# Kernel optimization log

Measured on AMD Instinct MI355X. Metric: run time of the kernel, lower is better.

The kernel has to match this reference:

```python
import jax, jax.numpy as jnp
import numpy as np

N = 50000
E = 800000
C_IN = 128
C_HID = 256
C_OUT = 128


def _glorot(key, shape):
    fan_in, fan_out = shape[0], shape[1]
    lim = (6.0 / (fan_in + fan_out)) ** 0.5
    return jax.random.uniform(key, shape, jnp.float32, -lim, lim)


def setup_inputs() -> dict:
    key = jax.random.key(0)
    ks = jax.random.split(key, 12)
    z = jax.random.normal(ks[0], (N, C_IN), jnp.float32)
    edge_index = jax.random.randint(ks[1], (2, E), 0, N, jnp.int64)
    edge_attr = jax.random.normal(ks[2], (E, 1), jnp.float32)
    # attr_decoder: Linear(C_IN+1 -> C_HID), ReLU, Linear(C_HID -> C_OUT)
    Wa1 = _glorot(ks[3], (C_IN + 1, C_HID))
    ba1 = jnp.zeros((C_HID,), jnp.float32)
    Wa2 = _glorot(ks[4], (C_HID, C_OUT))
    ba2 = jnp.zeros((C_OUT,), jnp.float32)
    # edge_decoder: Linear(2*C_IN -> C_HID), ReLU, Linear(C_HID -> 1)
    We1 = _glorot(ks[5], (2 * C_IN, C_HID))
    be1 = jnp.zeros((C_HID,), jnp.float32)
    We2 = _glorot(ks[6], (C_HID, 1))
    be2 = jnp.zeros((1,), jnp.float32)
    return {"z": z, "edge_index": edge_index, "edge_attr": edge_attr,
            "Wa1": Wa1, "ba1": ba1, "Wa2": Wa2, "ba2": ba2,
            "We1": We1, "be1": be1, "We2": We2, "be2": be2}


def reference(z, edge_index, edge_attr, Wa1, ba1, Wa2, ba2, We1, be1, We2, be2):
    src, dst = edge_index[0], edge_index[1]
    z_src = z[src]                                   # [E, C_IN] gather
    z_dst = z[dst]                                   # [E, C_IN] gather
    # edge decoder MLP on concatenated endpoint features
    edge_input = jnp.concatenate([z_src, z_dst], axis=-1)        # [E, 2*C_IN]
    h_e = jax.nn.relu(edge_input @ We1 + be1)                    # [E, C_HID]
    edge_recon = h_e @ We2 + be2                                 # [E, 1]
    # scatter_mean of cat([edge_attr, z_src]) over dst -> [N, C_IN+1]
    msg = jnp.concatenate([edge_attr, z_src], axis=1)            # [E, C_IN+1]
    seg_sum = jax.ops.segment_sum(msg, dst, num_segments=N)      # [N, C_IN+1]
    counts = jax.ops.segment_sum(jnp.ones((msg.shape[0],), msg.dtype), dst,
                                 num_segments=N)                  # [N]
    struct_ctx = jnp.where(counts[:, None] > 0,
                           seg_sum / jnp.maximum(counts[:, None], 1.0), 0.0)
    # node attribute decoder MLP
    h_a = jax.nn.relu(struct_ctx @ Wa1 + ba1)                    # [N, C_HID]
    x_recon = h_a @ Wa2 + ba2                                    # [N, C_OUT]
    return (x_recon, edge_recon)
```

## Files before the change

### kernel.cpp

```cpp
#include <hip/hip_runtime.h>

#define N_NODES 50000
#define N_EDGES 800000
#define C_IN    128
#define C_HID   256
#define C_OUT   128
#define YSTRIDE 512

typedef __bf16 bf16x8 __attribute__((ext_vector_type(8)));
typedef float  f32x4  __attribute__((ext_vector_type(4)));

__device__ __forceinline__ unsigned short f2bf(float x) {
    unsigned u = __float_as_uint(x);
    u = (u + 0x7FFF + ((u >> 16) & 1)) >> 16;
    return (unsigned short)u;
}

__global__ __launch_bounds__(256) void prep_kernel(
    const float* __restrict__ z, const int* __restrict__ ei,
    const float* __restrict__ We1, const float* __restrict__ Wa1,
    const float* __restrict__ Wa2,
    unsigned short* __restrict__ zb, int* __restrict__ cnt, int* __restrict__ epos,
    unsigned short* __restrict__ Bpack, unsigned short* __restrict__ Wa1b,
    unsigned short* __restrict__ Wa2b)
{
    const int b = blockIdx.x;
    const int tid = threadIdx.x;
    if (b < 6250) {
        int t = b * 256 + tid;
        float4 v = ((const float4*)z)[t];
        ushort4 o;
        o.x = f2bf(v.x); o.y = f2bf(v.y); o.z = f2bf(v.z); o.w = f2bf(v.w);
        ((ushort4*)zb)[t] = o;
    } else if (b < 6250 + 3125) {
        int e = (b - 6250) * 256 + tid;
        epos[e] = atomicAdd(&cnt[ei[N_EDGES + e]], 1);
    } else if (b < 6250 + 3125 + 32) {
        int t = (b - 6250 - 3125) * 256 + tid;
        int lane = t & 63, nt = (t >> 6) & 15, ks = t >> 10;
        int n  = nt * 16 + (lane & 15);
        int kb = ks * 32 + (lane >> 4) * 8;
        #pragma unroll
        for (int j = 0; j < 8; ++j)
            Bpack[t * 8 + j] = f2bf(We1[(kb + j) * C_HID + n]);
    } else if (b < 6250 + 3125 + 32 + 20) {
        int t = (b - 6250 - 3125 - 32) * 256 + tid;
        if (t >= 5 * 16 * 64) return;
        int lane = t & 63, nt = (t >> 6) & 15, ks = t >> 10;
        int n = nt * 16 + (lane & 15);
        #pragma unroll
        for (int j = 0; j < 8; ++j) {
            int k = ks * 32 + (lane >> 4) * 8 + j;
            float v = 0.f;
            if (k < 128)       v = Wa1[(k + 1) * C_HID + n];
            else if (k == 128) v = Wa1[0 * C_HID + n];
            Wa1b[t * 8 + j] = f2bf(v);
        }
    } else {
        int t = (b - 6250 - 3125 - 32 - 20) * 256 + tid;
        if (t >= 8 * 8 * 64) return;
        int lane = t & 63, nt = (t >> 6) & 7, ks = t >> 9;
        int n  = nt * 16 + (lane & 15);
        int kb = ks * 32 + (lane >> 4) * 8;
        #pragma unroll
        for (int j = 0; j < 8; ++j)
            Wa2b[t * 8 + j] = f2bf(Wa2[(kb + j) * C_OUT + n]);
    }
}

__global__ __launch_bounds__(1024) void scan_kernel(const int* __restrict__ cnt,
                                                    int* __restrict__ offsets) {
    const int tid = threadIdx.x;
    const int base = tid * 49;
    int c[49];
    int sum = 0;
    #pragma unroll
    for (int i = 0; i < 49; ++i) { c[i] = cnt[base + i]; sum += c[i]; }
    const int lane = tid & 63, w = tid >> 6;
    int v = sum;
    #pragma unroll
    for (int off = 1; off < 64; off <<= 1) {
        int t = __shfl_up(v, off, 64);
        if (lane >= off) v += t;
    }
    __shared__ int s_w[16];
    if (lane == 63) s_w[w] = v;
    __syncthreads();
    int wbase = 0;
    #pragma unroll
    for (int i = 0; i < 16; ++i) wbase += (i < w) ? s_w[i] : 0;
    int run = wbase + v - sum;
    #pragma unroll
    for (int i = 0; i < 49; ++i) { offsets[base + i] = run; run += c[i]; }
}

__global__ __launch_bounds__(256, 2) void fy_kernel(
    const int* __restrict__ ei, const float* __restrict__ eattr,
    const int* __restrict__ offsets, const int* __restrict__ epos,
    int4* __restrict__ erec,
    const unsigned short* __restrict__ zb, const unsigned short* __restrict__ Bpack,
    const float* __restrict__ be1, unsigned short* __restrict__ Y)
{
    const int tid = threadIdx.x;
    if (blockIdx.x >= 1564) {
        int e = (blockIdx.x - 1564) * 256 + tid;
        int d = ei[N_EDGES + e];
        erec[offsets[d] + epos[e]] = make_int4(ei[e], e, __float_as_int(eattr[e]), 0);
        return;
    }
    __shared__ __align__(16) unsigned short s_a[64][136];
    const int yb = blockIdx.x;
    const int n0 = (yb >> 1) * 64;
    const int half = yb & 1;
    const int lane = tid & 63, w = tid >> 6;
    const int m16 = lane & 15, quad = lane >> 4;

    #pragma unroll
    for (int i = 0; i < 4; ++i) {
        int c = tid + i * 256;
        int row = c >> 4, col = (c & 15) * 8;
        *(uint4*)&s_a[row][col] = *(const uint4*)(zb + (size_t)(n0 + row) * C_IN + col);
    }

    bf16x8 bfr[4][4];
    {
        const bf16x8* bp = (const bf16x8*)Bpack;
        #pragma unroll
        for (int ks = 0; ks < 4; ++ks)
            #pragma unroll
            for (int nt = 0; nt < 4; ++nt)
                bfr[ks][nt] = bp[((half * 4 + ks) * 16 + (w * 4 + nt)) * 64 + lane];
    }
    __syncthreads();

    f32x4 acc[4][4];
    #pragma unroll
    for (int mt = 0; mt < 4; ++mt)
        #pragma unroll
        for (int nt = 0; nt < 4; ++nt)
            acc[mt][nt] = (f32x4){0.f, 0.f, 0.f, 0.f};

    #pragma unroll
    for (int ks = 0; ks < 4; ++ks) {
        #pragma unroll
        for (int mt = 0; mt < 4; ++mt) {
            bf16x8 a = *(const bf16x8*)&s_a[mt * 16 + m16][ks * 32 + quad * 8];
            #pragma unroll
            for (int nt = 0; nt < 4; ++nt)
                acc[mt][nt] = __builtin_amdgcn_mfma_f32_16x16x32_bf16(
                    a, bfr[ks][nt], acc[mt][nt], 0, 0, 0);
        }
    }

    #pragma unroll
    for (int nt = 0; nt < 4; ++nt) {
        const int c = w * 64 + nt * 16 + m16;
        const float b = half ? be1[c] : 0.f;
        #pragma unroll
        for (int mt = 0; mt < 4; ++mt)
            #pragma unroll
            for (int r = 0; r < 4; ++r) {
                const int node = n0 + mt * 16 + quad * 4 + r;
                Y[(size_t)node * YSTRIDE + half * 256 + c] = f2bf(acc[mt][nt][r] + b);
            }
    }
}

__device__ __forceinline__ float dot8(uint4 q, const float* __restrict__ d,
                                      const float* __restrict__ wv, float p) {
    const unsigned u[4] = {q.x, q.y, q.z, q.w};
    #pragma unroll
    for (int j = 0; j < 4; ++j) {
        const float lo = __uint_as_float(u[j] << 16)         + d[2 * j];
        const float hi = __uint_as_float(u[j] & 0xffff0000u) + d[2 * j + 1];
        p = fmaf(fmaxf(lo, 0.f), wv[2 * j],     p);
        p = fmaf(fmaxf(hi, 0.f), wv[2 * j + 1], p);
    }
    return p;
}

__global__ __launch_bounds__(64, 6) void fused_eg_kernel(
    unsigned short* __restrict__ Y, const unsigned short* __restrict__ zb,
    const int* __restrict__ offsets, const int4* __restrict__ erec,
    const float* __restrict__ We2, const float* __restrict__ be2,
    float* __restrict__ edge_out)
{
    const int lane = threadIdx.x;
    const int n = blockIdx.x;
    const int c = lane & 15, g = lane >> 4;
    const int beg = offsets[n], end = offsets[n + 1], deg = end - beg;
    const float be2v = be2[0];

    float d0[8], d1[8], w0[8], w1[8];
    {
        const unsigned short* yh = Y + (size_t)n * YSTRIDE + 256;
        uint4 q0 = *(const uint4*)(yh + c * 8);
        uint4 q1 = *(const uint4*)(yh + 128 + c * 8);
        const unsigned a0[4] = {q0.x, q0.y, q0.z, q0.w};
        const unsigned a1[4] = {q1.x, q1.y, q1.z, q1.w};
        #pragma unroll
        for (int j = 0; j < 4; ++j) {
            d0[2 * j]     = __uint_as_float(a0[j] << 16);
            d0[2 * j + 1] = __uint_as_float(a0[j] & 0xffff0000u);
            d1[2 * j]     = __uint_as_float(a1[j] << 16);
            d1[2 * j + 1] = __uint_as_float(a1[j] & 0xffff0000u);
        }
        #pragma unroll
        for (int j = 0; j < 8; ++j) {
            w0[j] = We2[c * 8 + j];
            w1[j] = We2[128 + c * 8 + j];
        }
    }

    float ax = 0.f, ay = 0.f;
    float asum = 0.f;
    const int nfull = deg >> 2;
    int i = beg;
    int4 ra, rb, rc, rd;
    if (nfull) { ra = erec[i]; rb = erec[i + 1]; rc = erec[i + 2]; rd = erec[i + 3]; }
    for (int it = 0; it < nfull; ++it) {
        const int4 c0 = ra, c1 = rb, c2 = rc, c3 = rd;
        i += 4;
        if (it + 1 < nfull) {
            ra = erec[i]; rb = erec[i + 1]; rc = erec[i + 2]; rd = erec[i + 3];
        }
        asum += __int_as_float(c0.z) + __int_as_float(c1.z)
              + __int_as_float(c2.z) + __int_as_float(c3.z);
        const unsigned u0 = *(const unsigned*)(zb + (size_t)c0.x * C_IN + lane * 2);
        const unsigned u1 = *(const unsigned*)(zb + (size_t)c1.x * C_IN + lane * 2);
        const unsigned u2 = *(const unsigned*)(zb + (size_t)c2.x * C_IN + lane * 2);
        const unsigned u3 = *(const unsigned*)(zb + (size_t)c3.x * C_IN + lane * 2);
        ax += __uint_as_float(u0 << 16) + __uint_as_float(u1 << 16)
            + __uint_as_float(u2 << 16) + __uint_as_float(u3 << 16);
        ay += __uint_as_float(u0 & 0xffff0000u) + __uint_as_float(u1 & 0xffff0000u)
            + __uint_as_float(u2 & 0xffff0000u) + __uint_as_float(u3 & 0xffff0000u);
        const int sg = (g == 0) ? c0.x : (g == 1) ? c1.x : (g == 2) ? c2.x : c3.x;
        const int eg = (g == 0) ? c0.y : (g == 1) ? c1.y : (g == 2) ? c2.y : c3.y;
        const unsigned short* yr = Y + (size_t)sg * YSTRIDE;
        const uint4 q0 = *(const uint4*)(yr + c * 8);
        const uint4 q1 = *(const uint4*)(yr + 128 + c * 8);
        float p = dot8(q0, d0, w0, 0.f);
        p = dot8(q1, d1, w1, p);
        p += __shfl_xor(p, 1, 64);
        p += __shfl_xor(p, 2, 64);
        p += __shfl_xor(p, 4, 64);
        p += __shfl_xor(p, 8, 64);
        if (c == 0) edge_out[eg] = p + be2v;
    }
    for (; i < end; ++i) {
        const int4 r = erec[i];
        asum += __int_as_float(r.z);
        const unsigned u = *(const unsigned*)(zb + (size_t)r.x * C_IN + lane * 2);
        ax += __uint_as_float(u << 16);
        ay += __uint_as_float(u & 0xffff0000u);
        const unsigned short* yr = Y + (size_t)r.x * YSTRIDE;
        const uint4 q0 = *(const uint4*)(yr + c * 8);
        const uint4 q1 = *(const uint4*)(yr + 128 + c * 8);
        float p = dot8(q0, d0, w0, 0.f);
        p = dot8(q1, d1, w1, p);
        p += __shfl_xor(p, 1, 64);
        p += __shfl_xor(p, 2, 64);
        p += __shfl_xor(p, 4, 64);
        p += __shfl_xor(p, 8, 64);
        if (lane == 0) edge_out[r.y] = p + be2v;
    }

    const float inv = (deg > 0) ? 1.0f / (float)deg : 0.0f;
    unsigned short* segn = Y + (size_t)n * YSTRIDE + 256;
    ushort2 o; o.x = f2bf(ax * inv); o.y = f2bf(ay * inv);
    *(ushort2*)(segn + lane * 2) = o;
    if (lane < 16) {
        ushort2 pz; pz.x = (lane == 0) ? f2bf(asum * inv) : (unsigned short)0; pz.y = 0;
        *(ushort2*)(segn + 128 + lane * 2) = pz;
    }
}

__global__ __launch_bounds__(256, 2) void node_mfma_kernel(
    const unsigned short* __restrict__ segb, const unsigned short* __restrict__ Wa1b,
    const float* __restrict__ ba1, const unsigned short* __restrict__ Wa2b,
    const float* __restrict__ ba2, float* __restrict__ x_out)
{
    __shared__ __align__(16) unsigned short s_a[64][168];
    __shared__ __align__(16) unsigned short s_h[64][264];
    const int tid  = threadIdx.x;
    const int lane = tid & 63, w = tid >> 6;
    const int m16 = lane & 15, quad = lane >> 4;
    const int n0 = blockIdx.x * 64;

    {
        const unsigned short* src = segb + (size_t)n0 * YSTRIDE + 256;
        #pragma unroll
        for (int i = 0; i < 5; ++i) {
            int c = tid + i * 256;
            int row = c / 20, col = c - row * 20;
            *(uint4*)&s_a[row][col * 8] =
                *(const uint4*)(src + (size_t)row * YSTRIDE + col * 8);
        }
    }

    bf16x8 bfr1[5][4];
    {
        const bf16x8* bp = (const bf16x8*)Wa1b;
        #pragma unroll
        for (int ks = 0; ks < 5; ++ks)
            #pragma unroll
            for (int nt = 0; nt < 4; ++nt)
                bfr1[ks][nt] = bp[(ks * 16 + (w * 4 + nt)) * 64 + lane];
    }
    __syncthreads();

    f32x4 acc1[4][4];
    #pragma unroll
    for (int mt = 0; mt < 4; ++mt)
        #pragma unroll
        for (int nt = 0; nt < 4; ++nt)
            acc1[mt][nt] = (f32x4){0.f, 0.f, 0.f, 0.f};

    #pragma unroll
    for (int ks = 0; ks < 5; ++ks) {
        #pragma unroll
        for (int mt = 0; mt < 4; ++mt) {
            bf16x8 a = *(const bf16x8*)&s_a[mt * 16 + m16][ks * 32 + quad * 8];
            #pragma unroll
            for (int nt = 0; nt < 4; ++nt)
                acc1[mt][nt] = __builtin_amdgcn_mfma_f32_16x16x32_bf16(
                    a, bfr1[ks][nt], acc1[mt][nt], 0, 0, 0);
        }
    }

    #pragma unroll
    for (int nt = 0; nt < 4; ++nt) {
        const int chan = w * 64 + nt * 16 + m16;
        const float b1 = ba1[chan];
        #pragma unroll
        for (int mt = 0; mt < 4; ++mt)
            #pragma unroll
            for (int r = 0; r < 4; ++r) {
                const int node = mt * 16 + quad * 4 + r;
                s_h[node][chan] = f2bf(fmaxf(acc1[mt][nt][r] + b1, 0.f));
            }
    }

    bf16x8 bfr2[8][2];
    {
        const bf16x8* bp = (const bf16x8*)Wa2b;
        #pragma unroll
        for (int ks = 0; ks < 8; ++ks)
            #pragma unroll
            for (int nt = 0; nt < 2; ++nt)
                bfr2[ks][nt] = bp[(ks * 8 + (w * 2 + nt)) * 64 + lane];
    }
    __syncthreads();

    f32x4 acc2[4][2];
    #pragma unroll
    for (int mt = 0; mt < 4; ++mt)
        #pragma unroll
        for (int nt = 0; nt < 2; ++nt)
            acc2[mt][nt] = (f32x4){0.f, 0.f, 0.f, 0.f};

    #pragma unroll
    for (int ks = 0; ks < 8; ++ks) {
        #pragma unroll
        for (int mt = 0; mt < 4; ++mt) {
            bf16x8 a = *(const bf16x8*)&s_h[mt * 16 + m16][ks * 32 + quad * 8];
            #pragma unroll
            for (int nt = 0; nt < 2; ++nt)
                acc2[mt][nt] = __builtin_amdgcn_mfma_f32_16x16x32_bf16(
                    a, bfr2[ks][nt], acc2[mt][nt], 0, 0, 0);
        }
    }

    #pragma unroll
    for (int nt = 0; nt < 2; ++nt) {
        const int j = w * 32 + nt * 16 + m16;
        const float b2 = ba2[j];
        #pragma unroll
        for (int mt = 0; mt < 4; ++mt)
            #pragma unroll
            for (int r = 0; r < 4; ++r) {
                const int node = n0 + mt * 16 + quad * 4 + r;
                if (node < N_NODES)
                    x_out[(size_t)node * C_OUT + j] = acc2[mt][nt][r] + b2;
            }
    }
}


extern "C" void kernel_launch(void* const* d_in, const int* in_sizes, int n_in,
                              void* d_out, int out_size, void* d_ws, size_t ws_size,
                              hipStream_t stream) {
    const float* z     = (const float*)d_in[0];
    const int*   ei    = (const int*)d_in[1];
    const float* eattr = (const float*)d_in[2];
    const float* Wa1   = (const float*)d_in[3];
    const float* ba1   = (const float*)d_in[4];
    const float* Wa2   = (const float*)d_in[5];
    const float* ba2   = (const float*)d_in[6];
    const float* We1   = (const float*)d_in[7];
    const float* be1   = (const float*)d_in[8];
    const float* We2   = (const float*)d_in[9];
    const float* be2   = (const float*)d_in[10];

    float* x_out    = (float*)d_out;
    float* edge_out = x_out + (size_t)N_NODES * C_OUT;

    char* wsb = (char*)d_ws;
    size_t off = 0;
    unsigned short* Y        = (unsigned short*)(wsb + off); off += 51249152;
    unsigned short* zb       = (unsigned short*)(wsb + off); off += 12812288;
    unsigned short* Bpack    = (unsigned short*)(wsb + off); off += 131072;
    unsigned short* Wa1b     = (unsigned short*)(wsb + off); off += 81920;
    unsigned short* Wa2b     = (unsigned short*)(wsb + off); off += 65536;
    int*            cnt      = (int*)(wsb + off);            off += 200704;
    int*            offsets  = (int*)(wsb + off);            off += 200704;
    int*            epos     = (int*)(wsb + off);            off += 3200000;
    int4*           erec     = (int4*)(wsb + off);           off += 12800000;

    hipMemsetAsync(cnt, 0, 200704, stream);

    prep_kernel<<<6250 + 3125 + 32 + 20 + 16, 256, 0, stream>>>(
        z, ei, We1, Wa1, Wa2, zb, cnt, epos, Bpack, Wa1b, Wa2b);

    scan_kernel<<<1, 1024, 0, stream>>>(cnt, offsets);

    fy_kernel<<<1564 + 3125, 256, 0, stream>>>(ei, eattr, offsets, epos, erec,
                                               zb, Bpack, be1, Y);

    fused_eg_kernel<<<N_NODES, 64, 0, stream>>>(
        Y, zb, offsets, erec, We2, be2, edge_out);

    node_mfma_kernel<<<(N_NODES + 63) / 64, 256, 0, stream>>>(Y, Wa1b, ba1, Wa2b,
                                                              ba2, x_out);
}
```

Measured before the change: 302.9 us.

## Pack edge records to 8 bytes and pad segments to multiples of four

Edge records shrink from int4 to int2 by packing the 16-bit source index with a bf16 copy of the edge attribute, which halves record traffic. Each node's segment is padded to a multiple of four in the scan, so the scalar tail loop disappears and padded slots are masked out. The padding is zeroed by extending the memset over the record buffer. The trade-offs are reduced precision on the edge attribute and a larger memset, and the source index only fits because N is below 65536.

```diff
diff --git a/kernel.cpp b/kernel.cpp
--- a/kernel.cpp
+++ b/kernel.cpp
@@ -14,6 +14,9 @@
     unsigned u = __float_as_uint(x);
     u = (u + 0x7FFF + ((u >> 16) & 1)) >> 16;
     return (unsigned short)u;
+}
+__device__ __forceinline__ float bf2f(unsigned short h) {
+    return __uint_as_float((unsigned)h << 16);
 }
 
 __global__ __launch_bounds__(256) void prep_kernel(
@@ -75,7 +78,10 @@
     int c[49];
     int sum = 0;
     #pragma unroll
-    for (int i = 0; i < 49; ++i) { c[i] = cnt[base + i]; sum += c[i]; }
+    for (int i = 0; i < 49; ++i) {
+        int cv = (cnt[base + i] + 3) & ~3;
+        c[i] = cv; sum += cv;
+    }
     const int lane = tid & 63, w = tid >> 6;
     int v = sum;
     #pragma unroll
@@ -97,7 +103,7 @@
 __global__ __launch_bounds__(256, 2) void fy_kernel(
     const int* __restrict__ ei, const float* __restrict__ eattr,
     const int* __restrict__ offsets, const int* __restrict__ epos,
-    int4* __restrict__ erec,
+    int2* __restrict__ erec,
     const unsigned short* __restrict__ zb, const unsigned short* __restrict__ Bpack,
     const float* __restrict__ be1, unsigned short* __restrict__ Y)
 {
@@ -105,7 +111,9 @@
     if (blockIdx.x >= 1564) {
         int e = (blockIdx.x - 1564) * 256 + tid;
         int d = ei[N_EDGES + e];
-        erec[offsets[d] + epos[e]] = make_int4(ei[e], e, __float_as_int(eattr[e]), 0);
+        unsigned ab = f2bf(eattr[e]);
+        erec[offsets[d] + epos[e]] =
+            make_int2((int)((unsigned)ei[e] | (ab << 16)), e);
         return;
     }
     __shared__ __align__(16) unsigned short s_a[64][136];
@@ -181,14 +189,18 @@
 
 __global__ __launch_bounds__(64, 6) void fused_eg_kernel(
     unsigned short* __restrict__ Y, const unsigned short* __restrict__ zb,
-    const int* __restrict__ offsets, const int4* __restrict__ erec,
+    const int* __restrict__ offsets, const int* __restrict__ cnt,
+    const int2* __restrict__ erec,
     const float* __restrict__ We2, const float* __restrict__ be2,
     float* __restrict__ edge_out)
 {
     const int lane = threadIdx.x;
     const int n = blockIdx.x;
     const int c = lane & 15, g = lane >> 4;
-    const int beg = offsets[n], end = offsets[n + 1], deg = end - beg;
+    const int beg = offsets[n];
+    const int deg = cnt[n];
+    const int end = beg + deg;
+    const int ngrp = (deg + 3) >> 2;
     const float be2v = be2[0];
 
     float d0[8], d1[8], w0[8], w1[8];
@@ -214,27 +226,37 @@
 
     float ax = 0.f, ay = 0.f;
     float asum = 0.f;
-    const int nfull = deg >> 2;
     int i = beg;
-    int4 ra, rb, rc, rd;
-    if (nfull) { ra = erec[i]; rb = erec[i + 1]; rc = erec[i + 2]; rd = erec[i + 3]; }
-    for (int it = 0; it < nfull; ++it) {
-        const int4 c0 = ra, c1 = rb, c2 = rc, c3 = rd;
+    int2 ra, rb, rc, rd;
+    if (ngrp) { ra = erec[i]; rb = erec[i + 1]; rc = erec[i + 2]; rd = erec[i + 3]; }
+    for (int it = 0; it < ngrp; ++it) {
+        const int2 c0 = ra, c1 = rb, c2 = rc, c3 = rd;
+        const int i0 = i;
         i += 4;
-        if (it + 1 < nfull) {
+        if (it + 1 < ngrp) {
             ra = erec[i]; rb = erec[i + 1]; rc = erec[i + 2]; rd = erec[i + 3];
         }
-        asum += __int_as_float(c0.z) + __int_as_float(c1.z)
-              + __int_as_float(c2.z) + __int_as_float(c3.z);
-        const unsigned u0 = *(const unsigned*)(zb + (size_t)c0.x * C_IN + lane * 2);
-        const unsigned u1 = *(const unsigned*)(zb + (size_t)c1.x * C_IN + lane * 2);
-        const unsigned u2 = *(const unsigned*)(zb + (size_t)c2.x * C_IN + lane * 2);
-        const unsigned u3 = *(const unsigned*)(zb + (size_t)c3.x * C_IN + lane * 2);
+        const int s0 = c0.x & 0xffff, s1 = c1.x & 0xffff;
+        const int s2 = c2.x & 0xffff, s3 = c3.x & 0xffff;
+        asum += bf2f((unsigned short)((unsigned)c0.x >> 16))
+              + bf2f((unsigned short)((unsigned)c1.x >> 16))
+              + bf2f((unsigned short)((unsigned)c2.x >> 16))
+              + bf2f((unsigned short)((unsigned)c3.x >> 16));
+        unsigned u0 = *(const unsigned*)(zb + (size_t)s0 * C_IN + lane * 2);
+        unsigned u1 = *(const unsigned*)(zb + (size_t)s1 * C_IN + lane * 2);
+        unsigned u2 = *(const unsigned*)(zb + (size_t)s2 * C_IN + lane * 2);
+        unsigned u3 = *(const unsigned*)(zb + (size_t)s3 * C_IN + lane * 2);
+        if (it == ngrp - 1) {
+            const int rem = end - i0;
+            if (rem < 2) u1 = 0;
+            if (rem < 3) u2 = 0;
+            if (rem < 4) u3 = 0;
+        }
         ax += __uint_as_float(u0 << 16) + __uint_as_float(u1 << 16)
             + __uint_as_float(u2 << 16) + __uint_as_float(u3 << 16);
         ay += __uint_as_float(u0 & 0xffff0000u) + __uint_as_float(u1 & 0xffff0000u)
             + __uint_as_float(u2 & 0xffff0000u) + __uint_as_float(u3 & 0xffff0000u);
-        const int sg = (g == 0) ? c0.x : (g == 1) ? c1.x : (g == 2) ? c2.x : c3.x;
+        const int sg = (g == 0) ? s0 : (g == 1) ? s1 : (g == 2) ? s2 : s3;
         const int eg = (g == 0) ? c0.y : (g == 1) ? c1.y : (g == 2) ? c2.y : c3.y;
         const unsigned short* yr = Y + (size_t)sg * YSTRIDE;
         const uint4 q0 = *(const uint4*)(yr + c * 8);
@@ -245,24 +267,7 @@
         p += __shfl_xor(p, 2, 64);
         p += __shfl_xor(p, 4, 64);
         p += __shfl_xor(p, 8, 64);
-        if (c == 0) edge_out[eg] = p + be2v;
-    }
-    for (; i < end; ++i) {
-        const int4 r = erec[i];
-        asum += __int_as_float(r.z);
-        const unsigned u = *(const unsigned*)(zb + (size_t)r.x * C_IN + lane * 2);
-        ax += __uint_as_float(u << 16);
-        ay += __uint_as_float(u & 0xffff0000u);
-        const unsigned short* yr = Y + (size_t)r.x * YSTRIDE;
-        const uint4 q0 = *(const uint4*)(yr + c * 8);
-        const uint4 q1 = *(const uint4*)(yr + 128 + c * 8);
-        float p = dot8(q0, d0, w0, 0.f);
-        p = dot8(q1, d1, w1, p);
-        p += __shfl_xor(p, 1, 64);
-        p += __shfl_xor(p, 2, 64);
-        p += __shfl_xor(p, 4, 64);
-        p += __shfl_xor(p, 8, 64);
-        if (lane == 0) edge_out[r.y] = p + be2v;
+        if (c == 0 && i0 + g < end) edge_out[eg] = p + be2v;
     }
 
     const float inv = (deg > 0) ? 1.0f / (float)deg : 0.0f;
@@ -413,11 +418,11 @@
     unsigned short* Wa1b     = (unsigned short*)(wsb + off); off += 81920;
     unsigned short* Wa2b     = (unsigned short*)(wsb + off); off += 65536;
     int*            cnt      = (int*)(wsb + off);            off += 200704;
+    int2*           erec     = (int2*)(wsb + off);           off += 7600000;
     int*            offsets  = (int*)(wsb + off);            off += 200704;
     int*            epos     = (int*)(wsb + off);            off += 3200000;
-    int4*           erec     = (int4*)(wsb + off);           off += 12800000;
-
-    hipMemsetAsync(cnt, 0, 200704, stream);
+
+    hipMemsetAsync(cnt, 0, 200704 + 7600000, stream);
 
     prep_kernel<<<6250 + 3125 + 32 + 20 + 16, 256, 0, stream>>>(
         z, ei, We1, Wa1, Wa2, zb, cnt, epos, Bpack, Wa1b, Wa2b);
@@ -428,7 +433,7 @@
                                                zb, Bpack, be1, Y);
 
     fused_eg_kernel<<<N_NODES, 64, 0, stream>>>(
-        Y, zb, offsets, erec, We2, be2, edge_out);
+        Y, zb, offsets, cnt, erec, We2, be2, edge_out);
 
     node_mfma_kernel<<<(N_NODES + 63) / 64, 256, 0, stream>>>(Y, Wa1b, ba1, Wa2b,
                                                               ba2, x_out);
```

Measured after the change: 311.2 us. 2.8% more time.
